# Kernel tuning notes

Measured on AMD Instinct MI355X. Metric: run time of the kernel, lower is better.

The kernel has to match this reference:

```python
import jax, jax.numpy as jnp
import numpy as np

N_T, N_S, F_IN, H, N_OUT = 2048, 512, 7, 64, 3


def setup_inputs() -> dict:
    key = jax.random.key(0)
    ks = jax.random.split(key, 12)
    pts = jax.random.normal(ks[0], (N_T, 3), jnp.float32)
    centers = jax.random.normal(ks[1], (N_S, 3), jnp.float32)
    nrm = jax.random.normal(ks[2], (N_S, 3), jnp.float32)
    normals = nrm / jnp.linalg.norm(nrm, axis=-1, keepdims=True)
    areas = jax.random.uniform(ks[3], (N_S,), jnp.float32, 0.1, 1.0)
    ref_lengths = jax.random.uniform(ks[4], (2,), jnp.float32, 0.5, 1.5)

    def lin(k, i, o):
        return jax.random.normal(k, (i, o), jnp.float32) / np.float32(np.sqrt(i))

    return {
        "prediction_points": pts,
        "face_centers": centers,
        "face_normals": normals,
        "face_areas": areas,
        "reference_lengths": ref_lengths,
        "W1": lin(ks[5], F_IN, H), "b1": jnp.zeros((H,), jnp.float32),
        "W2": lin(ks[6], H, H),    "b2": jnp.zeros((H,), jnp.float32),
        "W3": lin(ks[7], H, H),    "b3": jnp.zeros((H,), jnp.float32),
        "Wout": lin(ks[8], H, N_OUT), "bout": jnp.zeros((N_OUT,), jnp.float32),
        "p_scale": jnp.float32(1.0), "p_bias": jnp.float32(0.0),
        "v_scale": jnp.float32(1.0), "v_bias": jnp.float32(0.0),
    }


def reference(prediction_points, face_centers, face_normals, face_areas,
              reference_lengths, W1, b1, W2, b2, W3, b3, Wout, bout,
              p_scale, p_bias, v_scale, v_bias):
    eps = jnp.float32(1e-8)
    # Pairwise relative geometry (translation/rotation-equivariant features).
    rvec = prediction_points[:, None, :] - face_centers[None, :, :]  # [T,S,3]
    r2 = jnp.sum(rvec * rvec, axis=-1)                               # [T,S]
    r = jnp.sqrt(r2 + eps)
    rhat = rvec / r[..., None]
    c = jnp.sum(rhat * face_normals[None, :, :], axis=-1)            # cos(angle)
    # Legendre polynomials P0..P3 (n_spherical_harmonics = 4).
    legendre = jnp.stack(
        [jnp.ones_like(c), c, 0.5 * (3.0 * c * c - 1.0),
         0.5 * (5.0 * c * c * c - 3.0 * c)], axis=-1)                # [T,S,4]
    # Multiscale nondimensional distance features, one per reference length.
    dfeat = 1.0 / (1.0 + r[..., None] / reference_lengths)           # [T,S,2]
    afeat = jnp.broadcast_to(jnp.log(face_areas)[None, :, None],
                             r.shape + (1,))                          # [T,S,1]
    feats = jnp.concatenate([dfeat, legendre, afeat], axis=-1)       # [T,S,7]
    # Kernel MLP evaluated per (target, source) pair.
    h = jnp.tanh(feats @ W1 + b1)
    h = jnp.tanh(h @ W2 + b2)
    h = jnp.tanh(h @ W3 + b3)
    out = h @ Wout + bout                                            # [T,S,3]
    # Green's-function-like decay, area-weighted boundary integral.
    decay = face_areas[None, :] / (r2 + 1.0)                         # [T,S]
    p = jnp.sum(out[..., 0] * decay, axis=1)                         # [T]
    vel = jnp.sum((out[..., 1:2] * rhat
                   + out[..., 2:3] * face_normals[None, :, :])
                  * decay[..., None], axis=1)                        # [T,3]
    pressure = p * p_scale + p_bias
    velocity = vel * v_scale + v_bias
    return jnp.concatenate([pressure[:, None], velocity], axis=-1)   # [T,4]
```

## Files before the change

### kernel.cpp

```cpp
#include <hip/hip_runtime.h>
#include <hip/hip_fp16.h>


#define N_T 2048
#define N_S 512
#define BLK 128
#define SCALE 2.885390081777927f

#define CPY_F 6400
#define CPY_V 1600

typedef _Float16 f16;
typedef _Float16 f16x8 __attribute__((ext_vector_type(8)));
typedef float f32x4 __attribute__((ext_vector_type(4)));
typedef unsigned short u16;
typedef unsigned int u32;

__device__ __forceinline__ float tanh_s(float x) {
    float e = __builtin_amdgcn_exp2f(x);
    return fmaf(-2.0f, __builtin_amdgcn_rcpf(e + 1.0f), 1.0f);
}

__device__ __forceinline__ f32x4 mfma16h(f16x8 a, f16x8 b, f32x4 c) {
    return __builtin_amdgcn_mfma_f32_16x16x32_f16(a, b, c, 0, 0, 0);
}

__device__ __forceinline__ u32 pkrtz(float a, float b) {
    return __builtin_bit_cast(u32, __builtin_amdgcn_cvt_pkrtz(a, b));
}

__device__ __forceinline__ void store4h(u16* dst, float t0, float t1, float t2, float t3) {
    uint2 w;
    w.x = pkrtz(t0, t1);
    w.y = pkrtz(t2, t3);
    *(uint2*)dst = w;
}

__global__ __launch_bounds__(256) void prep_kernel(
    const float* __restrict__ W1, const float* __restrict__ b1,
    const float* __restrict__ W2, const float* __restrict__ b2,
    const float* __restrict__ W3, const float* __restrict__ b3,
    const float* __restrict__ Wout, float* __restrict__ ws)
{
    const int tid = blockIdx.x * 256 + threadIdx.x;
    const int cpy = tid / 1792;
    const int rem = tid - cpy * 1792;
    const int fid = rem >> 6, lane = rem & 63;
    const int q = lane >> 4, l15 = lane & 15;

    if (fid < 24) {
        float x[8];
        bool lo = false;
        if (fid < 4) {
            const int mt = fid & 3;
            #pragma unroll
            for (int j = 0; j < 8; ++j)
                x[j] = (q == 0 && j < 7) ? W1[j * 64 + mt * 16 + l15] * SCALE : 0.f;
        } else if (fid < 12) {
            const int k = fid - 4, ks = k >> 2, mt = k & 3;
            #pragma unroll
            for (int j = 0; j < 8; ++j)
                x[j] = W2[(ks * 32 + q * 8 + j) * 64 + mt * 16 + l15] * SCALE;
        } else if (fid < 20) {
            const int k = fid - 12, ks = k >> 2, mt = k & 3;
            #pragma unroll
            for (int j = 0; j < 8; ++j)
                x[j] = W3[(ks * 32 + q * 8 + j) * 64 + mt * 16 + l15] * SCALE;
        } else {
            const int ks = fid & 1;
            lo = (fid >= 22);
            #pragma unroll
            for (int j = 0; j < 8; ++j)
                x[j] = (l15 < 3) ? Wout[(ks * 32 + q * 8 + j) * 3 + l15] : 0.f;
        }
        f16x8 v;
        #pragma unroll
        for (int j = 0; j < 8; ++j) {
            const f16 h = (f16)x[j];
            v[j] = lo ? (f16)(x[j] - (float)h) : h;
        }
        *(f16x8*)((char*)ws + (size_t)(cpy * CPY_V + fid * 64 + lane) * 16) = v;
    } else if (fid < 27) {
        const int Lb = fid - 24;
        float bv;
        if (Lb == 0)      bv = b1[lane];
        else if (Lb == 1) bv = b2[lane];
        else              bv = b3[lane];
        ws[cpy * CPY_F + 6144 + Lb * 64 + lane] = bv * SCALE;
    }
}

__global__ __launch_bounds__(BLK, 2) void globe_mfma(
    const float* __restrict__ pts, const float* __restrict__ ctr,
    const float* __restrict__ nrm, const float* __restrict__ areas,
    const float* __restrict__ rlen, const float* __restrict__ bout,
    const float* __restrict__ p_scale, const float* __restrict__ p_bias,
    const float* __restrict__ v_scale, const float* __restrict__ v_bias,
    const float* __restrict__ ws,
    float* __restrict__ out)
{
    __shared__ __align__(16) u16 hbuf[2][64][72];
    __shared__ float xr[4];

    const int tid  = threadIdx.x;
    const int lane = tid & 63;
    const int wv   = tid >> 6;
    const int l15  = lane & 15;
    const int q    = lane >> 4;
    const int t    = blockIdx.x;

    const f16x8* __restrict__ wsF0 = (const f16x8*)ws;
    const float4* __restrict__ wsB0 = (const float4*)(ws + 6144);
    float4 bias[12];
    #pragma unroll
    for (int L = 0; L < 3; ++L)
        #pragma unroll
        for (int mt = 0; mt < 4; ++mt)
            bias[L * 4 + mt] = wsB0[L * 16 + mt * 4 + q];
    const f16x8 oh0 = wsF0[20 * 64 + lane];
    const f16x8 oh1 = wsF0[21 * 64 + lane];
    const f16x8 ol0 = wsF0[22 * 64 + lane];
    const f16x8 ol1 = wsF0[23 * 64 + lane];

    const float px = pts[3 * t + 0], py = pts[3 * t + 1], pz = pts[3 * t + 2];
    const float invL0 = __builtin_amdgcn_rcpf(rlen[0]);
    const float invL1 = __builtin_amdgcn_rcpf(rlen[1]);
    f32x4 co_init = (f32x4){0.f, 0.f, 0.f, 0.f};
    if (q == 0) { co_init[0] = bout[0]; co_init[1] = bout[1]; co_init[2] = bout[2]; }

    u16 (*hb)[72] = hbuf[wv];
    const f16x8 fzero = (f16x8){0, 0, 0, 0, 0, 0, 0, 0};
    float accp = 0.f, avx = 0.f, avy = 0.f, avz = 0.f;

    #pragma unroll 1
    for (int ch = 0; ch < 4; ++ch) {
        const f16x8* __restrict__ wsFc = (const f16x8*)ws + ch * CPY_V;

        const int s = (wv * 4 + ch) * 64 + lane;
        const float cx = ctr[3 * s + 0], cy = ctr[3 * s + 1], cz = ctr[3 * s + 2];
        const float snx = nrm[3 * s + 0], sny = nrm[3 * s + 1], snz = nrm[3 * s + 2];
        const float ar = areas[s];
        const float rvx = px - cx, rvy = py - cy, rvz = pz - cz;
        const float r2 = rvx * rvx + rvy * rvy + rvz * rvz;
        const float r2e = r2 + 1e-8f;
        const float rinv = __builtin_amdgcn_rsqf(r2e);
        const float r = r2e * rinv;
        const float rhx = rvx * rinv, rhy = rvy * rinv, rhz = rvz * rinv;
        const float cth = rhx * snx + rhy * sny + rhz * snz;
        const float c2 = cth * cth;
        const float decay = ar * __builtin_amdgcn_rcpf(r2 + 1.0f);
        {
            uint4 fw;
            fw.x = pkrtz(__builtin_amdgcn_rcpf(fmaf(r, invL0, 1.0f)),
                         __builtin_amdgcn_rcpf(fmaf(r, invL1, 1.0f)));
            fw.y = pkrtz(1.0f, cth);
            fw.z = pkrtz(fmaf(1.5f, c2, -0.5f), cth * fmaf(2.5f, c2, -1.5f));
            fw.w = pkrtz(__logf(ar), 0.0f);
            *(uint4*)&hb[lane][0] = fw;
        }
        {
            uint4 g;
            g.x = __builtin_bit_cast(u32, decay);
            g.y = pkrtz(rhx, rhy);
            g.z = pkrtz(rhz, snx);
            g.w = pkrtz(sny, snz);
            *(uint4*)&hb[lane][64] = g;
        }

        {
            const f16x8 a0 = wsFc[0 * 64 + lane];
            const f16x8 a1 = wsFc[1 * 64 + lane];
            const f16x8 a2 = wsFc[2 * 64 + lane];
            const f16x8 a3 = wsFc[3 * 64 + lane];
            #pragma unroll
            for (int n4 = 0; n4 < 4; ++n4) {
                const int row = n4 * 16 + l15;
                const f16x8 lv = *(const f16x8*)&hb[row][0];
                const f16x8 bf = (q == 0) ? lv : fzero;
                f32x4 c[4];
                #pragma unroll
                for (int mt = 0; mt < 4; ++mt)
                    c[mt] = (f32x4){bias[mt].x, bias[mt].y, bias[mt].z, bias[mt].w};
                c[0] = mfma16h(a0, bf, c[0]);
                c[1] = mfma16h(a1, bf, c[1]);
                c[2] = mfma16h(a2, bf, c[2]);
                c[3] = mfma16h(a3, bf, c[3]);
                #pragma unroll
                for (int mt = 0; mt < 4; ++mt)
                    store4h(&hb[row][mt * 16 + q * 4],
                            tanh_s(c[mt][0]), tanh_s(c[mt][1]),
                            tanh_s(c[mt][2]), tanh_s(c[mt][3]));
            }
        }

        #pragma unroll
        for (int L = 0; L < 2; ++L) {
            const int fb = 4 + L * 8;
            const f16x8 a0 = wsFc[(fb + 0) * 64 + lane];
            const f16x8 a1 = wsFc[(fb + 1) * 64 + lane];
            const f16x8 a2 = wsFc[(fb + 2) * 64 + lane];
            const f16x8 a3 = wsFc[(fb + 3) * 64 + lane];
            const f16x8 a4 = wsFc[(fb + 4) * 64 + lane];
            const f16x8 a5 = wsFc[(fb + 5) * 64 + lane];
            const f16x8 a6 = wsFc[(fb + 6) * 64 + lane];
            const f16x8 a7 = wsFc[(fb + 7) * 64 + lane];
            #pragma unroll
            for (int n4 = 0; n4 < 4; ++n4) {
                const int row = n4 * 16 + l15;
                const f16x8 bfa = *(const f16x8*)&hb[row][q * 8];
                const f16x8 bfb = *(const f16x8*)&hb[row][32 + q * 8];
                f32x4 c[4];
                #pragma unroll
                for (int mt = 0; mt < 4; ++mt)
                    c[mt] = (f32x4){bias[(L + 1) * 4 + mt].x, bias[(L + 1) * 4 + mt].y,
                                    bias[(L + 1) * 4 + mt].z, bias[(L + 1) * 4 + mt].w};
                c[0] = mfma16h(a0, bfa, c[0]);
                c[1] = mfma16h(a1, bfa, c[1]);
                c[2] = mfma16h(a2, bfa, c[2]);
                c[3] = mfma16h(a3, bfa, c[3]);
                c[0] = mfma16h(a4, bfb, c[0]);
                c[1] = mfma16h(a5, bfb, c[1]);
                c[2] = mfma16h(a6, bfb, c[2]);
                c[3] = mfma16h(a7, bfb, c[3]);
                #pragma unroll
                for (int mt = 0; mt < 4; ++mt)
                    store4h(&hb[row][mt * 16 + q * 4],
                            tanh_s(c[mt][0]), tanh_s(c[mt][1]),
                            tanh_s(c[mt][2]), tanh_s(c[mt][3]));
            }
        }

        #pragma unroll
        for (int n4 = 0; n4 < 4; ++n4) {
            const int row = n4 * 16 + l15;
            const f16x8 bfa = *(const f16x8*)&hb[row][q * 8];
            const f16x8 bfb = *(const f16x8*)&hb[row][32 + q * 8];
            f32x4 co = co_init;
            co = mfma16h(oh0, bfa, co);
            co = mfma16h(ol0, bfa, co);
            co = mfma16h(oh1, bfb, co);
            co = mfma16h(ol1, bfb, co);
            if (q == 0) {
                const uint4 g = *(const uint4*)&hb[row][64];
                const float d = __builtin_bit_cast(float, g.x);
                const float2 rxy = __half22float2(__builtin_bit_cast(__half2, g.y));
                const float2 rzx = __half22float2(__builtin_bit_cast(__half2, g.z));
                const float2 nyz = __half22float2(__builtin_bit_cast(__half2, g.w));
                const float o0 = co[0], o1 = co[1], o2 = co[2];
                accp = fmaf(o0, d, accp);
                avx  = fmaf(fmaf(o1, rxy.x, o2 * rzx.y), d, avx);
                avy  = fmaf(fmaf(o1, rxy.y, o2 * nyz.x), d, avy);
                avz  = fmaf(fmaf(o1, rzx.x, o2 * nyz.y), d, avz);
            }
        }
    }

    #pragma unroll
    for (int off = 8; off > 0; off >>= 1) {
        accp += __shfl_down(accp, off);
        avx  += __shfl_down(avx,  off);
        avy  += __shfl_down(avy,  off);
        avz  += __shfl_down(avz,  off);
    }

    if (wv == 1 && lane == 0) {
        xr[0] = accp; xr[1] = avx; xr[2] = avy; xr[3] = avz;
    }
    __syncthreads();
    if (wv == 0 && lane == 0) {
        accp += xr[0]; avx += xr[1]; avy += xr[2]; avz += xr[3];
        const float ps = p_scale[0], pb = p_bias[0];
        const float vs = v_scale[0], vb = v_bias[0];
        out[4 * t + 0] = fmaf(accp, ps, pb);
        out[4 * t + 1] = fmaf(avx, vs, vb);
        out[4 * t + 2] = fmaf(avy, vs, vb);
        out[4 * t + 3] = fmaf(avz, vs, vb);
    }
}

extern "C" void kernel_launch(void* const* d_in, const int* in_sizes, int n_in,
                              void* d_out, int out_size, void* d_ws, size_t ws_size,
                              hipStream_t stream) {
    (void)in_sizes; (void)n_in; (void)ws_size; (void)out_size;
    const float* pts   = (const float*)d_in[0];
    const float* ctr   = (const float*)d_in[1];
    const float* nrm   = (const float*)d_in[2];
    const float* areas = (const float*)d_in[3];
    const float* rlen  = (const float*)d_in[4];
    const float* W1    = (const float*)d_in[5];
    const float* b1    = (const float*)d_in[6];
    const float* W2    = (const float*)d_in[7];
    const float* b2    = (const float*)d_in[8];
    const float* W3    = (const float*)d_in[9];
    const float* b3    = (const float*)d_in[10];
    const float* Wout  = (const float*)d_in[11];
    const float* bout  = (const float*)d_in[12];
    const float* ps    = (const float*)d_in[13];
    const float* pb    = (const float*)d_in[14];
    const float* vs    = (const float*)d_in[15];
    const float* vb    = (const float*)d_in[16];
    float* ws = (float*)d_ws;

    prep_kernel<<<28, 256, 0, stream>>>(W1, b1, W2, b2, W3, b3, Wout, ws);
    globe_mfma<<<N_T, BLK, 0, stream>>>(
        pts, ctr, nrm, areas, rlen, bout, ps, pb, vs, vb, ws, (float*)d_out);
}
```

Baseline: 149.9 us.

## Keep MLP activations in registers via 16x16x16 MFMA, dropping LDS round-trips

Switches from the 16x16x32 f16 MFMA to 16x16x16 so that each layer's output accumulator layout matches the next layer's B-operand layout. Hidden activations can then stay in registers between layers instead of being written to and read back from shared memory. The prep kernel repacks the weights into the matching fragment order, and biases are now reloaded from the workspace each chunk instead of being held in registers. The trade-offs are twice as many MFMA instructions and more register pressure from the B2/B3/BO fragment arrays and per-layer weight fragments, which could cost occupancy.

```diff
diff --git a/kernel.cpp b/kernel.cpp
--- a/kernel.cpp
+++ b/kernel.cpp
@@ -7,11 +7,11 @@
 #define BLK 128
 #define SCALE 2.885390081777927f
 
-#define CPY_F 6400
-#define CPY_V 1600
+#define CPY_F 5888
+#define CPY_U 1472
 
 typedef _Float16 f16;
-typedef _Float16 f16x8 __attribute__((ext_vector_type(8)));
+typedef _Float16 f16x4 __attribute__((ext_vector_type(4)));
 typedef float f32x4 __attribute__((ext_vector_type(4)));
 typedef unsigned short u16;
 typedef unsigned int u32;
@@ -21,19 +21,28 @@
     return fmaf(-2.0f, __builtin_amdgcn_rcpf(e + 1.0f), 1.0f);
 }
 
-__device__ __forceinline__ f32x4 mfma16h(f16x8 a, f16x8 b, f32x4 c) {
-    return __builtin_amdgcn_mfma_f32_16x16x32_f16(a, b, c, 0, 0, 0);
+__device__ __forceinline__ f32x4 mfma16(f16x4 a, f16x4 b, f32x4 c) {
+    return __builtin_amdgcn_mfma_f32_16x16x16f16(a, b, c, 0, 0, 0);
 }
 
 __device__ __forceinline__ u32 pkrtz(float a, float b) {
     return __builtin_bit_cast(u32, __builtin_amdgcn_cvt_pkrtz(a, b));
 }
 
-__device__ __forceinline__ void store4h(u16* dst, float t0, float t1, float t2, float t3) {
-    uint2 w;
-    w.x = pkrtz(t0, t1);
-    w.y = pkrtz(t2, t3);
-    *(uint2*)dst = w;
+__device__ __forceinline__ f16x4 lo4(uint4 g) {
+    uint2 p; p.x = g.x; p.y = g.y;
+    return __builtin_bit_cast(f16x4, p);
+}
+__device__ __forceinline__ f16x4 hi4(uint4 g) {
+    uint2 p; p.x = g.z; p.y = g.w;
+    return __builtin_bit_cast(f16x4, p);
+}
+
+__device__ __forceinline__ f16x4 tpack(f32x4 c) {
+    uint2 p;
+    p.x = pkrtz(tanh_s(c[0]), tanh_s(c[1]));
+    p.y = pkrtz(tanh_s(c[2]), tanh_s(c[3]));
+    return __builtin_bit_cast(f16x4, p);
 }
 
 __global__ __launch_bounds__(256) void prep_kernel(
@@ -43,50 +52,59 @@
     const float* __restrict__ Wout, float* __restrict__ ws)
 {
     const int tid = blockIdx.x * 256 + threadIdx.x;
-    const int cpy = tid / 1792;
-    const int rem = tid - cpy * 1792;
-    const int fid = rem >> 6, lane = rem & 63;
-    const int q = lane >> 4, l15 = lane & 15;
-
-    if (fid < 24) {
+    if (tid < 5632) {
+        const int cpy = tid / 1408;
+        const int r   = tid - cpy * 1408;
+        const int u   = r >> 6, lane = r & 63;
+        const int q = lane >> 4, l15 = lane & 15;
         float x[8];
         bool lo = false;
-        if (fid < 4) {
-            const int mt = fid & 3;
-            #pragma unroll
-            for (int j = 0; j < 8; ++j)
-                x[j] = (q == 0 && j < 7) ? W1[j * 64 + mt * 16 + l15] * SCALE : 0.f;
-        } else if (fid < 12) {
-            const int k = fid - 4, ks = k >> 2, mt = k & 3;
-            #pragma unroll
-            for (int j = 0; j < 8; ++j)
-                x[j] = W2[(ks * 32 + q * 8 + j) * 64 + mt * 16 + l15] * SCALE;
-        } else if (fid < 20) {
-            const int k = fid - 12, ks = k >> 2, mt = k & 3;
-            #pragma unroll
-            for (int j = 0; j < 8; ++j)
-                x[j] = W3[(ks * 32 + q * 8 + j) * 64 + mt * 16 + l15] * SCALE;
-        } else {
-            const int ks = fid & 1;
-            lo = (fid >= 22);
-            #pragma unroll
-            for (int j = 0; j < 8; ++j)
-                x[j] = (l15 < 3) ? Wout[(ks * 32 + q * 8 + j) * 3 + l15] : 0.f;
-        }
-        f16x8 v;
         #pragma unroll
-        for (int j = 0; j < 8; ++j) {
-            const f16 h = (f16)x[j];
-            v[j] = lo ? (f16)(x[j] - (float)h) : h;
-        }
-        *(f16x8*)((char*)ws + (size_t)(cpy * CPY_V + fid * 64 + lane) * 16) = v;
-    } else if (fid < 27) {
-        const int Lb = fid - 24;
+        for (int e = 0; e < 8; ++e) {
+            const int half = e >> 2, j = e & 3;
+            float v;
+            if (u < 2) {
+                const int mt = u * 2 + half;
+                const int k = q * 4 + j;
+                v = (k < 7) ? W1[k * 64 + mt * 16 + l15] * SCALE : 0.f;
+            } else if (u < 10) {
+                const int idx = u - 2, mt = idx >> 1, kp = idx & 1;
+                const int k = (kp * 2 + half) * 16 + q * 4 + j;
+                v = W2[k * 64 + mt * 16 + l15] * SCALE;
+            } else if (u < 18) {
+                const int idx = u - 10, mt = idx >> 1, kp = idx & 1;
+                const int k = (kp * 2 + half) * 16 + q * 4 + j;
+                v = W3[k * 64 + mt * 16 + l15] * SCALE;
+            } else {
+                const int kp = (u - 18) & 1;
+                const int k = (kp * 2 + half) * 16 + q * 4 + j;
+                v = (l15 < 3) ? Wout[k * 3 + l15] : 0.f;
+                lo = (u >= 20);
+            }
+            x[e] = v;
+        }
+        u16 outw[8];
+        #pragma unroll
+        for (int e = 0; e < 8; ++e) {
+            const f16 h = (f16)x[e];
+            const f16 val = lo ? (f16)(x[e] - (float)h) : h;
+            outw[e] = __builtin_bit_cast(u16, val);
+        }
+        uint4 g;
+        g.x = outw[0] | ((u32)outw[1] << 16);
+        g.y = outw[2] | ((u32)outw[3] << 16);
+        g.z = outw[4] | ((u32)outw[5] << 16);
+        g.w = outw[6] | ((u32)outw[7] << 16);
+        *(uint4*)((char*)ws + (size_t)cpy * CPY_F * 4 + (size_t)(u * 64 + lane) * 16) = g;
+    } else {
+        const int b = tid - 5632;
+        const int cpy = b / 192, i = b - cpy * 192;
+        const int Lb = i >> 6, j = i & 63;
         float bv;
-        if (Lb == 0)      bv = b1[lane];
-        else if (Lb == 1) bv = b2[lane];
-        else              bv = b3[lane];
-        ws[cpy * CPY_F + 6144 + Lb * 64 + lane] = bv * SCALE;
+        if (Lb == 0)      bv = b1[j];
+        else if (Lb == 1) bv = b2[j];
+        else              bv = b3[j];
+        ws[cpy * CPY_F + 5632 + i] = bv * SCALE;
     }
 }
 
@@ -99,7 +117,8 @@
     const float* __restrict__ ws,
     float* __restrict__ out)
 {
-    __shared__ __align__(16) u16 hbuf[2][64][72];
+    __shared__ __align__(16) u16 featL[2][64][8];
+    __shared__ __align__(16) uint4 geomL[2][64];
     __shared__ float xr[4];
 
     const int tid  = threadIdx.x;
@@ -107,20 +126,8 @@
     const int wv   = tid >> 6;
     const int l15  = lane & 15;
     const int q    = lane >> 4;
+    const int qf   = q & 1;
     const int t    = blockIdx.x;
-
-    const f16x8* __restrict__ wsF0 = (const f16x8*)ws;
-    const float4* __restrict__ wsB0 = (const float4*)(ws + 6144);
-    float4 bias[12];
-    #pragma unroll
-    for (int L = 0; L < 3; ++L)
-        #pragma unroll
-        for (int mt = 0; mt < 4; ++mt)
-            bias[L * 4 + mt] = wsB0[L * 16 + mt * 4 + q];
-    const f16x8 oh0 = wsF0[20 * 64 + lane];
-    const f16x8 oh1 = wsF0[21 * 64 + lane];
-    const f16x8 ol0 = wsF0[22 * 64 + lane];
-    const f16x8 ol1 = wsF0[23 * 64 + lane];
 
     const float px = pts[3 * t + 0], py = pts[3 * t + 1], pz = pts[3 * t + 2];
     const float invL0 = __builtin_amdgcn_rcpf(rlen[0]);
@@ -128,13 +135,15 @@
     f32x4 co_init = (f32x4){0.f, 0.f, 0.f, 0.f};
     if (q == 0) { co_init[0] = bout[0]; co_init[1] = bout[1]; co_init[2] = bout[2]; }
 
-    u16 (*hb)[72] = hbuf[wv];
-    const f16x8 fzero = (f16x8){0, 0, 0, 0, 0, 0, 0, 0};
+    u16 (*ft)[8] = featL[wv];
+    uint4* gp = geomL[wv];
+    const f16x4 bz = (f16x4){0, 0, 0, 0};
     float accp = 0.f, avx = 0.f, avy = 0.f, avz = 0.f;
 
     #pragma unroll 1
     for (int ch = 0; ch < 4; ++ch) {
-        const f16x8* __restrict__ wsFc = (const f16x8*)ws + ch * CPY_V;
+        const uint4* __restrict__ wsU = (const uint4*)ws + ch * CPY_U;
+        const float* __restrict__ wsBias = ws + ch * CPY_F + 5632;
 
         const int s = (wv * 4 + ch) * 64 + lane;
         const float cx = ctr[3 * s + 0], cy = ctr[3 * s + 1], cz = ctr[3 * s + 2];
@@ -156,7 +165,7 @@
             fw.y = pkrtz(1.0f, cth);
             fw.z = pkrtz(fmaf(1.5f, c2, -0.5f), cth * fmaf(2.5f, c2, -1.5f));
             fw.w = pkrtz(__logf(ar), 0.0f);
-            *(uint4*)&hb[lane][0] = fw;
+            *(uint4*)&ft[lane][0] = fw;
         }
         {
             uint4 g;
@@ -164,93 +173,122 @@
             g.y = pkrtz(rhx, rhy);
             g.z = pkrtz(rhz, snx);
             g.w = pkrtz(sny, snz);
-            *(uint4*)&hb[lane][64] = g;
-        }
-
-        {
-            const f16x8 a0 = wsFc[0 * 64 + lane];
-            const f16x8 a1 = wsFc[1 * 64 + lane];
-            const f16x8 a2 = wsFc[2 * 64 + lane];
-            const f16x8 a3 = wsFc[3 * 64 + lane];
+            gp[lane] = g;
+        }
+
+        f16x4 B2[4][4];
+        {
+            const uint4 g0 = wsU[0 * 64 + lane], g1 = wsU[1 * 64 + lane];
+            f16x4 a1[4];
+            a1[0] = lo4(g0); a1[1] = hi4(g0); a1[2] = lo4(g1); a1[3] = hi4(g1);
+            float4 bv[4];
+            #pragma unroll
+            for (int mt = 0; mt < 4; ++mt)
+                bv[mt] = *(const float4*)(wsBias + 0 * 64 + mt * 16 + q * 4);
             #pragma unroll
             for (int n4 = 0; n4 < 4; ++n4) {
-                const int row = n4 * 16 + l15;
-                const f16x8 lv = *(const f16x8*)&hb[row][0];
-                const f16x8 bf = (q == 0) ? lv : fzero;
+                const f16x4 lv = *(const f16x4*)&ft[n4 * 16 + l15][qf * 4];
+                const f16x4 bf = (q < 2) ? lv : bz;
                 f32x4 c[4];
                 #pragma unroll
-                for (int mt = 0; mt < 4; ++mt)
-                    c[mt] = (f32x4){bias[mt].x, bias[mt].y, bias[mt].z, bias[mt].w};
-                c[0] = mfma16h(a0, bf, c[0]);
-                c[1] = mfma16h(a1, bf, c[1]);
-                c[2] = mfma16h(a2, bf, c[2]);
-                c[3] = mfma16h(a3, bf, c[3]);
-                #pragma unroll
-                for (int mt = 0; mt < 4; ++mt)
-                    store4h(&hb[row][mt * 16 + q * 4],
-                            tanh_s(c[mt][0]), tanh_s(c[mt][1]),
-                            tanh_s(c[mt][2]), tanh_s(c[mt][3]));
-            }
-        }
-
-        #pragma unroll
-        for (int L = 0; L < 2; ++L) {
-            const int fb = 4 + L * 8;
-            const f16x8 a0 = wsFc[(fb + 0) * 64 + lane];
-            const f16x8 a1 = wsFc[(fb + 1) * 64 + lane];
-            const f16x8 a2 = wsFc[(fb + 2) * 64 + lane];
-            const f16x8 a3 = wsFc[(fb + 3) * 64 + lane];
-            const f16x8 a4 = wsFc[(fb + 4) * 64 + lane];
-            const f16x8 a5 = wsFc[(fb + 5) * 64 + lane];
-            const f16x8 a6 = wsFc[(fb + 6) * 64 + lane];
-            const f16x8 a7 = wsFc[(fb + 7) * 64 + lane];
+                for (int mt = 0; mt < 4; ++mt) {
+                    c[mt] = (f32x4){bv[mt].x, bv[mt].y, bv[mt].z, bv[mt].w};
+                    c[mt] = mfma16(a1[mt], bf, c[mt]);
+                }
+                #pragma unroll
+                for (int mt = 0; mt < 4; ++mt)
+                    B2[mt][n4] = tpack(c[mt]);
+            }
+        }
+
+        f16x4 B3[4][4];
+        {
+            f16x4 a[4][4];
+            #pragma unroll
+            for (int mt = 0; mt < 4; ++mt) {
+                const uint4 ga = wsU[(2 + 2 * mt) * 64 + lane];
+                const uint4 gb = wsU[(3 + 2 * mt) * 64 + lane];
+                a[mt][0] = lo4(ga); a[mt][1] = hi4(ga);
+                a[mt][2] = lo4(gb); a[mt][3] = hi4(gb);
+            }
+            float4 bv[4];
+            #pragma unroll
+            for (int mt = 0; mt < 4; ++mt)
+                bv[mt] = *(const float4*)(wsBias + 1 * 64 + mt * 16 + q * 4);
             #pragma unroll
             for (int n4 = 0; n4 < 4; ++n4) {
-                const int row = n4 * 16 + l15;
-                const f16x8 bfa = *(const f16x8*)&hb[row][q * 8];
-                const f16x8 bfb = *(const f16x8*)&hb[row][32 + q * 8];
                 f32x4 c[4];
                 #pragma unroll
                 for (int mt = 0; mt < 4; ++mt)
-                    c[mt] = (f32x4){bias[(L + 1) * 4 + mt].x, bias[(L + 1) * 4 + mt].y,
-                                    bias[(L + 1) * 4 + mt].z, bias[(L + 1) * 4 + mt].w};
-                c[0] = mfma16h(a0, bfa, c[0]);
-                c[1] = mfma16h(a1, bfa, c[1]);
-                c[2] = mfma16h(a2, bfa, c[2]);
-                c[3] = mfma16h(a3, bfa, c[3]);
-                c[0] = mfma16h(a4, bfb, c[0]);
-                c[1] = mfma16h(a5, bfb, c[1]);
-                c[2] = mfma16h(a6, bfb, c[2]);
-                c[3] = mfma16h(a7, bfb, c[3]);
-                #pragma unroll
-                for (int mt = 0; mt < 4; ++mt)
-                    store4h(&hb[row][mt * 16 + q * 4],
-                            tanh_s(c[mt][0]), tanh_s(c[mt][1]),
-                            tanh_s(c[mt][2]), tanh_s(c[mt][3]));
-            }
-        }
-
-        #pragma unroll
-        for (int n4 = 0; n4 < 4; ++n4) {
-            const int row = n4 * 16 + l15;
-            const f16x8 bfa = *(const f16x8*)&hb[row][q * 8];
-            const f16x8 bfb = *(const f16x8*)&hb[row][32 + q * 8];
-            f32x4 co = co_init;
-            co = mfma16h(oh0, bfa, co);
-            co = mfma16h(ol0, bfa, co);
-            co = mfma16h(oh1, bfb, co);
-            co = mfma16h(ol1, bfb, co);
-            if (q == 0) {
-                const uint4 g = *(const uint4*)&hb[row][64];
-                const float d = __builtin_bit_cast(float, g.x);
-                const float2 rxy = __half22float2(__builtin_bit_cast(__half2, g.y));
-                const float2 rzx = __half22float2(__builtin_bit_cast(__half2, g.z));
-                const float2 nyz = __half22float2(__builtin_bit_cast(__half2, g.w));
-                const float o0 = co[0], o1 = co[1], o2 = co[2];
-                accp = fmaf(o0, d, accp);
-                avx  = fmaf(fmaf(o1, rxy.x, o2 * rzx.y), d, avx);
-                avy  = fmaf(fmaf(o1, rxy.y, o2 * nyz.x), d, avy);
-                avz  = fmaf(fmaf(o1, rzx.x, o2 * nyz.y), d, avz);
+                    c[mt] = (f32x4){bv[mt].x, bv[mt].y, bv[mt].z, bv[mt].w};
+                #pragma unroll
+                for (int kt = 0; kt < 4; ++kt)
+                    #pragma unroll
+                    for (int mt = 0; mt < 4; ++mt)
+                        c[mt] = mfma16(a[mt][kt], B2[kt][n4], c[mt]);
+                #pragma unroll
+                for (int mt = 0; mt < 4; ++mt)
+                    B3[mt][n4] = tpack(c[mt]);
+            }
+        }
+
+        f16x4 BO[4][4];
+        {
+            f16x4 a[4][4];
+            #pragma unroll
+            for (int mt = 0; mt < 4; ++mt) {
+                const uint4 ga = wsU[(10 + 2 * mt) * 64 + lane];
+                const uint4 gb = wsU[(11 + 2 * mt) * 64 + lane];
+                a[mt][0] = lo4(ga); a[mt][1] = hi4(ga);
+                a[mt][2] = lo4(gb); a[mt][3] = hi4(gb);
+            }
+            float4 bv[4];
+            #pragma unroll
+            for (int mt = 0; mt < 4; ++mt)
+                bv[mt] = *(const float4*)(wsBias + 2 * 64 + mt * 16 + q * 4);
+            #pragma unroll
+            for (int n4 = 0; n4 < 4; ++n4) {
+                f32x4 c[4];
+                #pragma unroll
+                for (int mt = 0; mt < 4; ++mt)
+                    c[mt] = (f32x4){bv[mt].x, bv[mt].y, bv[mt].z, bv[mt].w};
+                #pragma unroll
+                for (int kt = 0; kt < 4; ++kt)
+                    #pragma unroll
+                    for (int mt = 0; mt < 4; ++mt)
+                        c[mt] = mfma16(a[mt][kt], B3[kt][n4], c[mt]);
+                #pragma unroll
+                for (int mt = 0; mt < 4; ++mt)
+                    BO[mt][n4] = tpack(c[mt]);
+            }
+        }
+
+        {
+            const uint4 gh0 = wsU[18 * 64 + lane], gh1 = wsU[19 * 64 + lane];
+            const uint4 gl0 = wsU[20 * 64 + lane], gl1 = wsU[21 * 64 + lane];
+            f16x4 aoh[4], aol[4];
+            aoh[0] = lo4(gh0); aoh[1] = hi4(gh0); aoh[2] = lo4(gh1); aoh[3] = hi4(gh1);
+            aol[0] = lo4(gl0); aol[1] = hi4(gl0); aol[2] = lo4(gl1); aol[3] = hi4(gl1);
+            #pragma unroll
+            for (int n4 = 0; n4 < 4; ++n4) {
+                f32x4 co = co_init;
+                #pragma unroll
+                for (int kt = 0; kt < 4; ++kt) {
+                    co = mfma16(aoh[kt], BO[kt][n4], co);
+                    co = mfma16(aol[kt], BO[kt][n4], co);
+                }
+                if (q == 0) {
+                    const uint4 g = gp[n4 * 16 + l15];
+                    const float d = __builtin_bit_cast(float, g.x);
+                    const float2 rxy = __half22float2(__builtin_bit_cast(__half2, g.y));
+                    const float2 rzx = __half22float2(__builtin_bit_cast(__half2, g.z));
+                    const float2 nyz = __half22float2(__builtin_bit_cast(__half2, g.w));
+                    const float o0 = co[0], o1 = co[1], o2 = co[2];
+                    accp = fmaf(o0, d, accp);
+                    avx  = fmaf(fmaf(o1, rxy.x, o2 * rzx.y), d, avx);
+                    avy  = fmaf(fmaf(o1, rxy.y, o2 * nyz.x), d, avy);
+                    avz  = fmaf(fmaf(o1, rzx.x, o2 * nyz.y), d, avz);
+                }
             }
         }
     }
@@ -301,7 +339,7 @@
     const float* vb    = (const float*)d_in[16];
     float* ws = (float*)d_ws;
 
-    prep_kernel<<<28, 256, 0, stream>>>(W1, b1, W2, b2, W3, b3, Wout, ws);
+    prep_kernel<<<25, 256, 0, stream>>>(W1, b1, W2, b2, W3, b3, Wout, ws);
     globe_mfma<<<N_T, BLK, 0, stream>>>(
         pts, ctr, nrm, areas, rlen, bout, ps, pb, vs, vb, ws, (float*)d_out);
 }
```

After: 154.6 us. 3.1% more time.
